# Optimization experiments

Hardware: AMD Instinct MI355X
Metric: run time of the kernel (lower is better)

The kernel has to match this reference:

```python
import jax, jax.numpy as jnp
import numpy as np

N, M, C, IN, OUT = 65536, 512, 512, 256, 256
EPS = 1e-8


def setup_inputs() -> dict:
    key = jax.random.key(0)
    ks = jax.random.split(key, 12)
    d = {}
    d["x"] = jax.random.normal(ks[0], (1, IN), jnp.float32)
    d["memory"] = jax.random.normal(ks[1], (1, N, M), jnp.float32) * 0.05
    d["prev_read"] = jax.random.normal(ks[2], (1, M), jnp.float32) * 0.05
    d["h"] = jnp.ones((1, C), jnp.float32)
    d["c"] = jnp.ones((1, C), jnp.float32)
    d["read_state"] = jnp.zeros((1, N), jnp.float32)
    d["write_state"] = jnp.zeros((1, N), jnp.float32)
    d["W_ih"] = jax.random.normal(ks[3], (4 * C, IN + M), jnp.float32) * 0.02
    d["b_ih"] = jax.random.normal(ks[4], (4 * C,), jnp.float32) * 0.01
    d["W_hh"] = jax.random.normal(ks[5], (4 * C, C), jnp.float32) * 0.02
    d["b_hh"] = jax.random.normal(ks[6], (4 * C,), jnp.float32) * 0.01
    d["W_read"] = jax.random.normal(ks[7], (M + 6, C), jnp.float32) * 0.02
    d["b_read"] = jnp.zeros((M + 6,), jnp.float32)
    d["W_write"] = jax.random.normal(ks[8], (3 * M + 6, C), jnp.float32) * 0.02
    d["b_write"] = jnp.zeros((3 * M + 6,), jnp.float32)
    d["W_out"] = jax.random.normal(ks[9], (OUT, C + M), jnp.float32) * 0.02
    d["b_out"] = jnp.zeros((OUT,), jnp.float32)
    return d


def _address(head_out, w_prev, memory):
    # head_out: [B, M+6(+...)]; returns sharpened addressing weights [B, N]
    key_v = head_out[:, :M]
    beta = jax.nn.softplus(head_out[:, M:M + 1])          # [B,1]
    g = jax.nn.sigmoid(head_out[:, M + 1:M + 2])          # [B,1]
    shift = jax.nn.softmax(head_out[:, M + 2:M + 5], axis=1)  # [B,3]
    gamma = 1.0 + jax.nn.softplus(head_out[:, M + 5:M + 6])   # [B,1]
    # content addressing: cosine similarity over memory rows
    a = memory + EPS                                      # [B,N,M]
    b = key_v[:, None, :] + EPS                           # [B,1,M]
    dot = jnp.sum(a * b, axis=-1)                         # [B,N]
    na = jnp.maximum(jnp.sqrt(jnp.sum(a * a, axis=-1)), EPS)
    nb = jnp.maximum(jnp.sqrt(jnp.sum(b * b, axis=-1)), EPS)
    cos = dot / (na * nb)
    w_context = jax.nn.softmax(beta * cos, axis=1)        # [B,N]
    # NOTE: original code swaps args -> g gates the PREVIOUS weights
    w_interp = g * w_prev + (1.0 - g) * w_context
    # circular shift via 3-tap correlation (conv1d with circular pad)
    w_pad = jnp.concatenate([w_interp[:, -1:], w_interp, w_interp[:, :1]], axis=1)
    w_shift = (w_pad[:, :-2] * shift[:, 0:1]
               + w_pad[:, 1:-1] * shift[:, 1:2]
               + w_pad[:, 2:] * shift[:, 2:3])
    power = w_shift ** gamma
    return power / (jnp.sum(power, axis=1, keepdims=True) + EPS)


def reference(x, memory, prev_read, h, c, read_state, write_state,
              W_ih, b_ih, W_hh, b_hh, W_read, b_read, W_write, b_write,
              W_out, b_out):
    # LSTMCell controller (torch gate order: i, f, g, o)
    inp = jnp.concatenate([x, prev_read], axis=1)                   # [B, IN+M]
    gates = inp @ W_ih.T + b_ih + h @ W_hh.T + b_hh                 # [B, 4C]
    i_g, f_g, g_g, o_g = jnp.split(gates, 4, axis=1)
    c_new = jax.nn.sigmoid(f_g) * c + jax.nn.sigmoid(i_g) * jnp.tanh(g_g)
    h_new = jax.nn.sigmoid(o_g) * jnp.tanh(c_new)

    # read head
    r_out = h_new @ W_read.T + b_read
    w_r = _address(r_out, read_state, memory)                       # [B,N]
    # faithful to torch.matmul([B,N],[B,N,M]).sum(1): sums weights over batch
    read = jnp.einsum('n,bnm->bm', jnp.sum(w_r, axis=0), memory)    # [B,M]

    # write head
    w_out_head = h_new @ W_write.T + b_write
    w_w = _address(w_out_head, write_state, memory)                 # [B,N]
    erase = jax.nn.sigmoid(w_out_head[:, M + 6:2 * M + 6])          # [B,M]
    add = w_out_head[:, 2 * M + 6:3 * M + 6]                        # [B,M]
    memory_new = memory * (1.0 - w_w[:, :, None] * erase[:, None, :]) \
                 + w_w[:, :, None] * add[:, None, :]                # [B,N,M]

    out = jax.nn.sigmoid(jnp.concatenate([h_new, read], axis=1) @ W_out.T + b_out)
    del memory_new  # state update; torch forward returns only the output
    return out
```

## Files before the change

### kernel.cpp

```cpp
#include <hip/hip_runtime.h>
#include <math.h>

#define EPS 1e-8f
#define NN 65536
#define MAGIC 1.0f

#define WS_GATES 0
#define WS_HNEW  2048
#define WS_ROUT  2560
#define WS_PMAX  3104
#define WS_PEXP  5152
#define WS_S     7200
#define WS_PSUM  72736
#define WS_PART  72992
#define WS_FLAGG 204064
#define WS_FLAGP 204192

__device__ __forceinline__ float wave_sum(float v) {
    for (int o = 32; o > 0; o >>= 1) v += __shfl_xor(v, o);
    return v;
}
__device__ __forceinline__ float sigm(float x) { return 1.f / (1.f + expf(-x)); }
__device__ __forceinline__ float softplusf_(float x) {
    return x > 20.f ? x : log1pf(expf(x));
}
__device__ __forceinline__ float dot4(float4 a, float4 b) {
    return a.x * b.x + a.y * b.y + a.z * b.z + a.w * b.w;
}
__device__ __forceinline__ float4 ld4(const float* p) { return *(const float4*)p; }

__device__ __forceinline__ float ald(const float* p) {
    return __hip_atomic_load(p, __ATOMIC_RELAXED, __HIP_MEMORY_SCOPE_AGENT);
}
__device__ __forceinline__ float ald_acq(const float* p) {
    return __hip_atomic_load(p, __ATOMIC_ACQUIRE, __HIP_MEMORY_SCOPE_AGENT);
}
__device__ __forceinline__ void ast(float* p, float v) {
    __hip_atomic_store(p, v, __ATOMIC_RELAXED, __HIP_MEMORY_SCOPE_AGENT);
}
__device__ __forceinline__ void ast_rel(float* p, float v) {
    __hip_atomic_store(p, v, __ATOMIC_RELEASE, __HIP_MEMORY_SCOPE_AGENT);
}
__device__ __forceinline__ float2 ald2(const float* p) {
    unsigned long long u = __hip_atomic_load((const unsigned long long*)p,
        __ATOMIC_RELAXED, __HIP_MEMORY_SCOPE_AGENT);
    float2 r; __builtin_memcpy(&r, &u, 8); return r;
}
__device__ __forceinline__ void ast2(float* p, float2 v) {
    unsigned long long u; __builtin_memcpy(&u, &v, 8);
    __hip_atomic_store((unsigned long long*)p, u,
        __ATOMIC_RELAXED, __HIP_MEMORY_SCOPE_AGENT);
}

__global__ __launch_bounds__(256) void k_front(const float* __restrict__ x,
                                               const float* __restrict__ pr,
                                               const float* __restrict__ h,
                                               const float* __restrict__ c,
                                               const float* __restrict__ W_ih,
                                               const float* __restrict__ b_ih,
                                               const float* __restrict__ W_hh,
                                               const float* __restrict__ b_hh,
                                               const float* __restrict__ W_read,
                                               const float* __restrict__ b_read,
                                               float* __restrict__ ws) {
    const int b = blockIdx.x, t = threadIdx.x;
    const int lane = t & 63, wv = t >> 6;
    __shared__ float sh[512];

    if (b < 128) {
        #pragma unroll
        for (int i = 0; i < 4; ++i) {
            const int row = b * 16 + wv * 4 + i;
            const float* wi = W_ih + (size_t)row * 768;
            const float* wh = W_hh + (size_t)row * 512;
            float acc = dot4(ld4(wi + lane * 4), ld4(x + lane * 4))
                      + dot4(ld4(wi + 256 + lane * 4), ld4(pr + lane * 4))
                      + dot4(ld4(wi + 512 + lane * 4), ld4(pr + 256 + lane * 4))
                      + dot4(ld4(wh + lane * 4), ld4(h + lane * 4))
                      + dot4(ld4(wh + 256 + lane * 4), ld4(h + 256 + lane * 4));
            acc = wave_sum(acc);
            if (lane == 0) ast(ws + WS_GATES + row, acc + b_ih[row] + b_hh[row]);
        }
        __syncthreads();
        if (t == 0) ast_rel(ws + WS_FLAGG + b, MAGIC);
    }

    if (wv == 0) {
        int cap = 0;
        for (;;) {
            float v0 = ald_acq(ws + WS_FLAGG + lane);
            float v1 = ald_acq(ws + WS_FLAGG + 64 + lane);
            if (__all(v0 == MAGIC && v1 == MAGIC)) break;
            __builtin_amdgcn_s_sleep(1);
            if (++cap > (1 << 20)) break;
        }
    }
    __syncthreads();

    for (int j = t; j < 512; j += 256) {
        float ig = ald(ws + WS_GATES + j);
        float fg = ald(ws + WS_GATES + 512 + j);
        float gg = ald(ws + WS_GATES + 1024 + j);
        float og = ald(ws + WS_GATES + 1536 + j);
        float cn = sigm(fg) * c[j] + sigm(ig) * tanhf(gg);
        float hn = sigm(og) * tanhf(cn);
        sh[j] = hn;
        if (b == 0) ws[WS_HNEW + j] = hn;
    }
    __syncthreads();
    const int o = b * 4 + wv;
    if (o < 518) {
        const float* wr = W_read + (size_t)o * 512;
        float acc = dot4(ld4(wr + lane * 4), ld4(sh + lane * 4))
                  + dot4(ld4(wr + 256 + lane * 4), ld4(sh + 256 + lane * 4));
        acc = wave_sum(acc);
        if (lane == 0) ws[WS_ROUT + o] = acc + b_read[o];
    }
}

__global__ __launch_bounds__(256) void k_cos(const float* __restrict__ mem,
                                             float* __restrict__ ws) {
    const int t = threadIdx.x, lane = t & 63, wv = t >> 6;
    const int gw = blockIdx.x * 4 + wv;
    const float* key = ws + WS_ROUT;
    float4 ka = ld4(key + lane * 4);
    float4 kb = ld4(key + 256 + lane * 4);
    ka.x += EPS; ka.y += EPS; ka.z += EPS; ka.w += EPS;
    kb.x += EPS; kb.y += EPS; kb.z += EPS; kb.w += EPS;
    float kq = wave_sum(dot4(ka, ka) + dot4(kb, kb));
    const float nb = fmaxf(sqrtf(kq), EPS);
    const float beta = softplusf_(key[512]);
    float* sp = ws + WS_S;
    float m = -1e30f, e = 0.f;
    for (int n = gw; n < NN; n += 8192) {
        float4 va = ld4(mem + (size_t)n * 512 + lane * 4);
        float4 vb = ld4(mem + (size_t)n * 512 + 256 + lane * 4);
        va.x += EPS; va.y += EPS; va.z += EPS; va.w += EPS;
        vb.x += EPS; vb.y += EPS; vb.z += EPS; vb.w += EPS;
        float dot = wave_sum(dot4(va, ka) + dot4(vb, kb));
        float sq  = wave_sum(dot4(va, va) + dot4(vb, vb));
        float na = fmaxf(sqrtf(sq), EPS);
        float sv = beta * dot / (na * nb);
        if (lane == 0) sp[n] = sv;
        float nm = fmaxf(m, sv);
        e = e * expf(m - nm) + expf(sv - nm);
        m = nm;
    }
    __shared__ float sm[4], se[4];
    if (lane == 0) { sm[wv] = m; se[wv] = e; }
    __syncthreads();
    if (t == 0) {
        float M = fmaxf(fmaxf(sm[0], sm[1]), fmaxf(sm[2], sm[3]));
        float E = se[0] * expf(sm[0] - M) + se[1] * expf(sm[1] - M) +
                  se[2] * expf(sm[2] - M) + se[3] * expf(sm[3] - M);
        ws[WS_PMAX + blockIdx.x] = M;
        ws[WS_PEXP + blockIdx.x] = E;
    }
}

__global__ __launch_bounds__(512) void k_readout(const float* __restrict__ mem,
                                                 const float* __restrict__ rs,
                                                 const float* __restrict__ W_out,
                                                 const float* __restrict__ b_out,
                                                 float* __restrict__ ws,
                                                 float* __restrict__ out) {
    const int b = blockIdx.x, t = threadIdx.x;
    const int lane = t & 63, wv = t >> 6;
    __shared__ float s_m[8], s_e[8];
    __shared__ float wi_l[258];
    __shared__ float pl[256];
    __shared__ float s_ps[4];
    __shared__ float4 sacc[3][128];
    __shared__ float rd[512];
    __shared__ float s_z[8];

    float m = -1e30f, e = 0.f;
    for (int i = t; i < 2048; i += 512) {
        float bm = ws[WS_PMAX + i], be = ws[WS_PEXP + i];
        float nm = fmaxf(m, bm);
        e = e * expf(m - nm) + be * expf(bm - nm);
        m = nm;
    }
    for (int o = 32; o > 0; o >>= 1) {
        float om = __shfl_xor(m, o), oe = __shfl_xor(e, o);
        float nm = fmaxf(m, om);
        e = e * expf(m - nm) + oe * expf(om - nm);
        m = nm;
    }
    if (lane == 0) { s_m[wv] = m; s_e[wv] = e; }
    __syncthreads();
    float mx = s_m[0];
    for (int i = 1; i < 8; ++i) mx = fmaxf(mx, s_m[i]);
    float Z = 0.f;
    for (int i = 0; i < 8; ++i) Z += s_e[i] * expf(s_m[i] - mx);
    const float invZ = 1.f / Z;
    const float g = sigm(ws[WS_ROUT + 513]);
    float a3 = ws[WS_ROUT + 514], b3 = ws[WS_ROUT + 515], c3 = ws[WS_ROUT + 516];
    float mm = fmaxf(a3, fmaxf(b3, c3));
    float ea = expf(a3 - mm), eb = expf(b3 - mm), ec = expf(c3 - mm);
    float ss = ea + eb + ec;
    const float s0 = ea / ss, s1 = eb / ss, s2 = ec / ss;
    const float gamma = 1.f + softplusf_(ws[WS_ROUT + 517]);

    const int start = b * 256;
    const float* sp = ws + WS_S;
    if (t < 258) {
        int idx = (start - 1 + t) & (NN - 1);
        wi_l[t] = g * rs[idx] + (1.f - g) * expf(sp[idx] - mx) * invZ;
    }
    __syncthreads();
    float ps = 0.f;
    if (t < 256) {
        float wsh = wi_l[t] * s0 + wi_l[t + 1] * s1 + wi_l[t + 2] * s2;
        float pv = powf(wsh, gamma);
        pl[t] = pv;
        ps = pv;
    }
    ps = wave_sum(ps);
    if (t < 256 && lane == 0) s_ps[wv] = ps;
    __syncthreads();
    if (t == 0) ast(ws + WS_PSUM + b, s_ps[0] + s_ps[1] + s_ps[2] + s_ps[3]);

    const int col = (t & 127) * 4;
    const int rq = t >> 7;
    float4 acc = make_float4(0.f, 0.f, 0.f, 0.f);
    const float* basep = mem + (size_t)start * 512 + col;
    #pragma unroll 8
    for (int r = rq; r < 256; r += 4) {
        float w = pl[r];
        float4 v = ld4(basep + (size_t)r * 512);
        acc.x += w * v.x; acc.y += w * v.y; acc.z += w * v.z; acc.w += w * v.w;
    }
    if (rq > 0) sacc[rq - 1][t & 127] = acc;
    __syncthreads();
    if (rq == 0) {
        float4 a0 = sacc[0][t & 127], a1 = sacc[1][t & 127], a2 = sacc[2][t & 127];
        acc.x += a0.x + a1.x + a2.x;
        acc.y += a0.y + a1.y + a2.y;
        acc.z += a0.z + a1.z + a2.z;
        acc.w += a0.w + a1.w + a2.w;
        float* pp = ws + WS_PART + (size_t)b * 512 + col;
        ast2(pp, make_float2(acc.x, acc.y));
        ast2(pp + 2, make_float2(acc.z, acc.w));
    }
    __syncthreads();
    if (t == 0) ast_rel(ws + WS_FLAGP + b, MAGIC);

    if (b >= 32) return;
    if (wv == 0) {
        int cap = 0;
        for (;;) {
            float v0 = ald_acq(ws + WS_FLAGP + lane);
            float v1 = ald_acq(ws + WS_FLAGP + 64 + lane);
            float v2 = ald_acq(ws + WS_FLAGP + 128 + lane);
            float v3 = ald_acq(ws + WS_FLAGP + 192 + lane);
            if (__all(v0 == MAGIC && v1 == MAGIC && v2 == MAGIC && v3 == MAGIC))
                break;
            __builtin_amdgcn_s_sleep(1);
            if (++cap > (1 << 20)) break;
        }
    }
    __syncthreads();
    float z = (t < 256) ? ald(ws + WS_PSUM + t) : 0.f;
    z = wave_sum(z);
    if (lane == 0) s_z[wv] = z;
    __syncthreads();
    float Zp = 0.f;
    for (int i = 0; i < 8; ++i) Zp += s_z[i];
    const float invZp = 1.f / (Zp + EPS);
    if (t < 256) {
        float ax = 0.f, ay = 0.f;
        const float* pp = ws + WS_PART + t * 2;
        #pragma unroll 16
        for (int r = 0; r < 256; ++r) {
            float2 v = ald2(pp + (size_t)r * 512);
            ax += v.x; ay += v.y;
        }
        rd[2 * t] = ax * invZp;
        rd[2 * t + 1] = ay * invZp;
    }
    __syncthreads();
    const int o = b * 8 + wv;
    const float* wo = W_out + (size_t)o * 1024;
    float a = dot4(ld4(wo + lane * 4), ld4(ws + WS_HNEW + lane * 4))
            + dot4(ld4(wo + 256 + lane * 4), ld4(ws + WS_HNEW + 256 + lane * 4))
            + dot4(ld4(wo + 512 + lane * 4), ld4(rd + lane * 4))
            + dot4(ld4(wo + 768 + lane * 4), ld4(rd + 256 + lane * 4));
    a = wave_sum(a);
    if (lane == 0) out[o] = sigm(a + b_out[o]);
}

extern "C" void kernel_launch(void* const* d_in, const int* in_sizes, int n_in,
                              void* d_out, int out_size, void* d_ws, size_t ws_size,
                              hipStream_t stream) {
    const float* x          = (const float*)d_in[0];
    const float* memory     = (const float*)d_in[1];
    const float* prev_read  = (const float*)d_in[2];
    const float* h          = (const float*)d_in[3];
    const float* c          = (const float*)d_in[4];
    const float* read_state = (const float*)d_in[5];
    const float* W_ih   = (const float*)d_in[7];
    const float* b_ih   = (const float*)d_in[8];
    const float* W_hh   = (const float*)d_in[9];
    const float* b_hh   = (const float*)d_in[10];
    const float* W_read = (const float*)d_in[11];
    const float* b_read = (const float*)d_in[12];
    const float* W_out  = (const float*)d_in[15];
    const float* b_out  = (const float*)d_in[16];
    float* ws  = (float*)d_ws;
    float* out = (float*)d_out;

    k_front<<<130, 256, 0, stream>>>(x, prev_read, h, c, W_ih, b_ih, W_hh, b_hh,
                                     W_read, b_read, ws);
    k_cos<<<2048, 256, 0, stream>>>(memory, ws);
    k_readout<<<256, 512, 0, stream>>>(memory, read_state, W_out, b_out, ws, out);
}
```

Before: 77.90 us.

## Stage bf16 copy of memory in cosine pass for cheaper weighted readout

While the cosine-similarity kernel streams each memory row, it also writes a bf16 copy of that row into the workspace. The readout kernel then accumulates the weighted row sum from the bf16 copy instead of rereading fp32 memory, which halves the bytes read in the second pass. The price is an extra bf16 write stream in the first pass, so total traffic stays about the same, and the read vector loses precision. The cosine kernel also interleaves the two wave reductions into a single shuffle loop.

Result: no change. 76.58 us (-1.7%).

```diff
diff --git a/kernel.cpp b/kernel.cpp
--- a/kernel.cpp
+++ b/kernel.cpp
@@ -15,6 +15,7 @@
 #define WS_PART  72992
 #define WS_FLAGG 204064
 #define WS_FLAGP 204192
+#define WS_BF    262144
 
 __device__ __forceinline__ float wave_sum(float v) {
     for (int o = 32; o > 0; o >>= 1) v += __shfl_xor(v, o);
@@ -50,6 +51,13 @@
     unsigned long long u; __builtin_memcpy(&u, &v, 8);
     __hip_atomic_store((unsigned long long*)p, u,
         __ATOMIC_RELAXED, __HIP_MEMORY_SCOPE_AGENT);
+}
+
+__device__ __forceinline__ unsigned bf2(float a, float b) {
+    unsigned ua = __float_as_uint(a), ub = __float_as_uint(b);
+    unsigned ra = (ua + 0x7FFFu + ((ua >> 16) & 1u)) >> 16;
+    unsigned rb = (ub + 0x7FFFu + ((ub >> 16) & 1u)) >> 16;
+    return ra | (rb << 16);
 }
 
 __global__ __launch_bounds__(256) void k_front(const float* __restrict__ x,
@@ -123,6 +131,7 @@
     const int t = threadIdx.x, lane = t & 63, wv = t >> 6;
     const int gw = blockIdx.x * 4 + wv;
     const float* key = ws + WS_ROUT;
+    unsigned short* wsb = (unsigned short*)(ws + WS_BF);
     float4 ka = ld4(key + lane * 4);
     float4 kb = ld4(key + 256 + lane * 4);
     ka.x += EPS; ka.y += EPS; ka.z += EPS; ka.w += EPS;
@@ -135,10 +144,18 @@
     for (int n = gw; n < NN; n += 8192) {
         float4 va = ld4(mem + (size_t)n * 512 + lane * 4);
         float4 vb = ld4(mem + (size_t)n * 512 + 256 + lane * 4);
+        uint2 p0 = make_uint2(bf2(va.x, va.y), bf2(va.z, va.w));
+        uint2 p1 = make_uint2(bf2(vb.x, vb.y), bf2(vb.z, vb.w));
+        *(uint2*)(wsb + (size_t)n * 512 + lane * 4) = p0;
+        *(uint2*)(wsb + (size_t)n * 512 + 256 + lane * 4) = p1;
         va.x += EPS; va.y += EPS; va.z += EPS; va.w += EPS;
         vb.x += EPS; vb.y += EPS; vb.z += EPS; vb.w += EPS;
-        float dot = wave_sum(dot4(va, ka) + dot4(vb, kb));
-        float sq  = wave_sum(dot4(va, va) + dot4(vb, vb));
+        float dot = dot4(va, ka) + dot4(vb, kb);
+        float sq  = dot4(va, va) + dot4(vb, vb);
+        for (int o = 32; o > 0; o >>= 1) {
+            dot += __shfl_xor(dot, o);
+            sq  += __shfl_xor(sq, o);
+        }
         float na = fmaxf(sqrtf(sq), EPS);
         float sv = beta * dot / (na * nb);
         if (lane == 0) sp[n] = sv;
@@ -158,8 +175,7 @@
     }
 }
 
-__global__ __launch_bounds__(512) void k_readout(const float* __restrict__ mem,
-                                                 const float* __restrict__ rs,
+__global__ __launch_bounds__(512) void k_readout(const float* __restrict__ rs,
                                                  const float* __restrict__ W_out,
                                                  const float* __restrict__ b_out,
                                                  float* __restrict__ ws,
@@ -170,7 +186,7 @@
     __shared__ float wi_l[258];
     __shared__ float pl[256];
     __shared__ float s_ps[4];
-    __shared__ float4 sacc[3][128];
+    __shared__ float sacc[8][512];
     __shared__ float rd[512];
     __shared__ float s_z[8];
 
@@ -221,27 +237,37 @@
     __syncthreads();
     if (t == 0) ast(ws + WS_PSUM + b, s_ps[0] + s_ps[1] + s_ps[2] + s_ps[3]);
 
-    const int col = (t & 127) * 4;
-    const int rq = t >> 7;
-    float4 acc = make_float4(0.f, 0.f, 0.f, 0.f);
-    const float* basep = mem + (size_t)start * 512 + col;
-    #pragma unroll 8
-    for (int r = rq; r < 256; r += 4) {
-        float w = pl[r];
-        float4 v = ld4(basep + (size_t)r * 512);
-        acc.x += w * v.x; acc.y += w * v.y; acc.z += w * v.z; acc.w += w * v.w;
-    }
-    if (rq > 0) sacc[rq - 1][t & 127] = acc;
-    __syncthreads();
-    if (rq == 0) {
-        float4 a0 = sacc[0][t & 127], a1 = sacc[1][t & 127], a2 = sacc[2][t & 127];
-        acc.x += a0.x + a1.x + a2.x;
-        acc.y += a0.y + a1.y + a2.y;
-        acc.z += a0.z + a1.z + a2.z;
-        acc.w += a0.w + a1.w + a2.w;
-        float* pp = ws + WS_PART + (size_t)b * 512 + col;
-        ast2(pp, make_float2(acc.x, acc.y));
-        ast2(pp + 2, make_float2(acc.z, acc.w));
+    {
+        const unsigned short* wsb = (const unsigned short*)(ws + WS_BF);
+        float a0 = 0.f, a1 = 0.f, a2 = 0.f, a3f = 0.f,
+              a4 = 0.f, a5 = 0.f, a6 = 0.f, a7 = 0.f;
+        #pragma unroll 4
+        for (int r = wv; r < 256; r += 8) {
+            float w = pl[r];
+            uint4 q = *(const uint4*)(wsb + (size_t)(start + r) * 512 + lane * 8);
+            a0 += w * __uint_as_float(q.x << 16);
+            a1 += w * __uint_as_float(q.x & 0xFFFF0000u);
+            a2 += w * __uint_as_float(q.y << 16);
+            a3f += w * __uint_as_float(q.y & 0xFFFF0000u);
+            a4 += w * __uint_as_float(q.z << 16);
+            a5 += w * __uint_as_float(q.z & 0xFFFF0000u);
+            a6 += w * __uint_as_float(q.w << 16);
+            a7 += w * __uint_as_float(q.w & 0xFFFF0000u);
+        }
+        float* sw = &sacc[wv][lane * 8];
+        sw[0] = a0; sw[1] = a1; sw[2] = a2; sw[3] = a3f;
+        sw[4] = a4; sw[5] = a5; sw[6] = a6; sw[7] = a7;
+    }
+    __syncthreads();
+    if (t < 256) {
+        const int cc = t * 2;
+        float u0 = 0.f, u1 = 0.f;
+        #pragma unroll
+        for (int w8 = 0; w8 < 8; ++w8) {
+            u0 += sacc[w8][cc];
+            u1 += sacc[w8][cc + 1];
+        }
+        ast2(ws + WS_PART + (size_t)b * 512 + cc, make_float2(u0, u1));
     }
     __syncthreads();
     if (t == 0) ast_rel(ws + WS_FLAGP + b, MAGIC);
@@ -313,5 +339,5 @@
     k_front<<<130, 256, 0, stream>>>(x, prev_read, h, c, W_ih, b_ih, W_hh, b_hh,
                                      W_read, b_read, ws);
     k_cos<<<2048, 256, 0, stream>>>(memory, ws);
-    k_readout<<<256, 512, 0, stream>>>(memory, read_state, W_out, b_out, ws, out);
-}
+    k_readout<<<256, 512, 0, stream>>>(read_state, W_out, b_out, ws, out);
+}
```
